# Kernel tuning notes

Hardware: AMD Instinct MI355X
Metric: run time of the kernel (lower is better)

Reference implementation:

```python
import jax, jax.numpy as jnp
import numpy as np

N_NODES = 50000
N_EDGES = 1600000
IN_CH = 128
HEADS = 4
HEAD_DIM = 32  # out_channels // heads = 128 // 4
NEG_SLOPE = 0.2


def setup_inputs() -> dict:
    key = jax.random.key(0)
    ks = jax.random.split(key, 6)
    x = jax.random.normal(ks[0], (N_NODES, IN_CH), dtype=jnp.float32)
    edge_index = jax.random.randint(ks[1], (2, N_EDGES), 0, N_NODES, dtype=jnp.int64)
    W = jax.random.normal(ks[2], (IN_CH, HEADS * HEAD_DIM), dtype=jnp.float32) * 0.1
    att_src = jax.random.normal(ks[3], (HEADS, HEAD_DIM), dtype=jnp.float32) * 0.1
    att_dst = jax.random.normal(ks[4], (HEADS, HEAD_DIM), dtype=jnp.float32) * 0.1
    bias = jax.random.normal(ks[5], (HEADS * HEAD_DIM,), dtype=jnp.float32) * 0.1
    return {"x": x, "edge_index": edge_index, "W": W,
            "att_src": att_src, "att_dst": att_dst, "bias": bias}


def reference(x, edge_index, W, att_src, att_dst, bias):
    N = x.shape[0]
    # linear projection, split heads: [N, H, C]
    h = (x @ W).reshape(N, HEADS, HEAD_DIM)
    # per-node attention logits: [N, H]
    a_src = jnp.einsum('nhc,hc->nh', h, att_src)
    a_dst = jnp.einsum('nhc,hc->nh', h, att_dst)
    # add self loops (PyG default)
    loops = jnp.arange(N, dtype=edge_index.dtype)
    src = jnp.concatenate([edge_index[0], loops])  # message source j
    dst = jnp.concatenate([edge_index[1], loops])  # message target i
    # edge attention scores: [E_total, H]
    alpha = jax.nn.leaky_relu(a_src[src] + a_dst[dst], NEG_SLOPE)
    # segment softmax over incoming edges per destination node
    amax = jax.ops.segment_max(alpha, dst, num_segments=N)
    alpha = jnp.exp(alpha - amax[dst])
    denom = jax.ops.segment_sum(alpha, dst, num_segments=N)
    alpha = alpha / (denom[dst] + 1e-16)
    # weighted scatter-aggregate: [N, H, C]
    msg = h[src] * alpha[:, :, None]
    out = jax.ops.segment_sum(msg, dst, num_segments=N)
    out = out.reshape(N, HEADS * HEAD_DIM) + bias
    return jax.nn.elu(out)
```

## Files before the change

### kernel.cpp

```cpp
#include <hip/hip_runtime.h>

typedef unsigned short u16;
typedef unsigned int u32;

#define CH 128
#define NHEAD 4
#define NEG_SLOPE 0.2f
#define ROWS_PER_BLOCK 32

#define LOG_NPB 7
#define NPB 128
#define NBMAX 400
#define BCAP 6144
#define KMAX 24
#define GPAD 16
#define BINA_BLOCKS 256

static __device__ __forceinline__ float bitf(u32 i) {
    float f; __builtin_memcpy(&f, &i, 4); return f;
}
static __device__ __forceinline__ float bflo(u32 v) { return bitf(v << 16); }
static __device__ __forceinline__ float bfhi(u32 v) { return bitf(v & 0xffff0000u); }
static __device__ __forceinline__ u16 f2bf(float f) {
    u32 i; __builtin_memcpy(&i, &f, 4);
    return (u16)((i + 0x7fffu + ((i >> 16) & 1u)) >> 16);
}
static __device__ __forceinline__ float lrelu(float v) { return v > 0.f ? v : NEG_SLOPE * v; }

static __device__ __forceinline__ int ei_at(const int* __restrict__ ei, int mode32, size_t idx) {
    return mode32 ? ei[idx] : ei[2 * idx];
}

__global__ __launch_bounds__(256) void gemmbin_kernel(
    const float* __restrict__ x, const float* __restrict__ W,
    const float* __restrict__ att_src, const float* __restrict__ att_dst,
    u16* __restrict__ h, float* __restrict__ asrc, float* __restrict__ adst, int N,
    const int* __restrict__ ei, int* __restrict__ gcur, u32* __restrict__ rec,
    int E, int NB)
{
    __shared__ u32 Wbf[CH][CH / 2];

    const int tid = threadIdx.x;

    if (blockIdx.x < BINA_BLOCKS) {
        int* hist  = (int*)&Wbf[0][0];
        int* hbase = hist + NBMAX;
        int* hcur  = hbase + NBMAX;
        const int mode32 = __syncthreads_or(ei[2 * tid + 1] != 0);
        for (int b = tid; b < NB; b += 256) { hist[b] = 0; hcur[b] = 0; }
        __syncthreads();
        const int chunk = (E + BINA_BLOCKS - 1) / BINA_BLOCKS;
        const int beg0 = blockIdx.x * chunk;
        const int end0 = min(E, beg0 + chunk);
#pragma unroll 4
        for (int e = beg0 + tid; e < end0; e += 256) {
            int dj = ei_at(ei, mode32, (size_t)E + e);
            atomicAdd(&hist[dj >> LOG_NPB], 1);
        }
        __syncthreads();
        for (int b = tid; b < NB; b += 256) {
            int c = hist[b];
            hbase[b] = c ? atomicAdd(&gcur[b * GPAD], c) : 0;
        }
        __syncthreads();
#pragma unroll 4
        for (int e = beg0 + tid; e < end0; e += 256) {
            int dj = ei_at(ei, mode32, (size_t)E + e);
            int sj = ei_at(ei, mode32, (size_t)e);
            int bkt = dj >> LOG_NPB;
            int r = atomicAdd(&hcur[bkt], 1);
            int pos = hbase[bkt] + r;
            if (pos < BCAP)
                rec[(size_t)bkt * BCAP + pos] = ((u32)sj << LOG_NPB) | (u32)(dj & (NPB - 1));
        }
        return;
    }

    const int gb = blockIdx.x - BINA_BLOCKS;
    const int r0b = gb * ROWS_PER_BLOCK;
#pragma unroll
    for (int i = 0; i < 16; ++i) {
        int f = tid + i * 256;
        int row = f >> 5;
        int col = (f & 31) * 4;
        float4 w4 = *(const float4*)(W + (size_t)row * CH + col);
        Wbf[row][(col >> 1)]     = (u32)f2bf(w4.x) | ((u32)f2bf(w4.y) << 16);
        Wbf[row][(col >> 1) + 1] = (u32)f2bf(w4.z) | ((u32)f2bf(w4.w) << 16);
    }
    __syncthreads();

    const int lane = tid & 63;
    const int wave = tid >> 6;
    const int c0 = lane * 2;
    const int head = lane >> 4;
    const float as0 = att_src[c0], as1 = att_src[c0 + 1];
    const float ad0 = att_dst[c0], ad1 = att_dst[c0 + 1];
    const int rwu = __builtin_amdgcn_readfirstlane(wave * 8);

    const float* xr[8];
#pragma unroll
    for (int r = 0; r < 8; ++r) {
        int row = r0b + rwu + r;
        row = row < N - 1 ? row : N - 1;
        xr[r] = x + (size_t)row * CH;
    }

    float acc[8][2];
#pragma unroll
    for (int r = 0; r < 8; ++r) { acc[r][0] = 0.f; acc[r][1] = 0.f; }

#pragma unroll 2
    for (int k4 = 0; k4 < 32; ++k4) {
        const int k = k4 * 4;
        u32 p0 = Wbf[k + 0][lane];
        u32 p1 = Wbf[k + 1][lane];
        u32 p2 = Wbf[k + 2][lane];
        u32 p3 = Wbf[k + 3][lane];
        float w00 = bflo(p0), w01 = bfhi(p0);
        float w10 = bflo(p1), w11 = bfhi(p1);
        float w20 = bflo(p2), w21 = bfhi(p2);
        float w30 = bflo(p3), w31 = bfhi(p3);
#pragma unroll
        for (int r = 0; r < 8; ++r) {
            float4 xv = *(const float4*)(xr[r] + k);
            acc[r][0] = fmaf(xv.x, w00, acc[r][0]);
            acc[r][1] = fmaf(xv.x, w01, acc[r][1]);
            acc[r][0] = fmaf(xv.y, w10, acc[r][0]);
            acc[r][1] = fmaf(xv.y, w11, acc[r][1]);
            acc[r][0] = fmaf(xv.z, w20, acc[r][0]);
            acc[r][1] = fmaf(xv.z, w21, acc[r][1]);
            acc[r][0] = fmaf(xv.w, w30, acc[r][0]);
            acc[r][1] = fmaf(xv.w, w31, acc[r][1]);
        }
    }
#pragma unroll
    for (int r = 0; r < 8; ++r) {
        int row = r0b + rwu + r;
        float sdot = acc[r][0] * as0 + acc[r][1] * as1;
        float ddot = acc[r][0] * ad0 + acc[r][1] * ad1;
#pragma unroll
        for (int o = 1; o < 16; o <<= 1) {
            sdot += __shfl_xor(sdot, o, 64);
            ddot += __shfl_xor(ddot, o, 64);
        }
        if (row < N) {
            u32 hp = (u32)f2bf(acc[r][0]) | ((u32)f2bf(acc[r][1]) << 16);
            *(u32*)(h + (size_t)row * CH + c0) = hp;
            if ((lane & 15) == 0) {
                asrc[row * NHEAD + head] = sdot;
                adst[row * NHEAD + head] = ddot;
            }
        }
    }
}

__global__ __launch_bounds__(256) void binB_kernel(
    const int* __restrict__ gcur, const u32* __restrict__ rec,
    int* __restrict__ csr, int* __restrict__ begA, int* __restrict__ degA, int N)
{
    __shared__ int outb[BCAP];
    __shared__ int lcnt[NPB];
    __shared__ int lsc[NPB];
    __shared__ int lcur[NPB];
    const int tid = threadIdx.x;
    const int bkt = blockIdx.x;
    int cnt0 = gcur[bkt * GPAD];
    cnt0 = cnt0 < BCAP ? cnt0 : BCAP;
    const size_t rbase = (size_t)bkt * BCAP;

    if (tid < NPB) { lcnt[tid] = 0; lcur[tid] = 0; }

    u32 rc[KMAX];
#pragma unroll
    for (int k = 0; k < KMAX; ++k) {
        int i = tid + k * 256;
        rc[k] = (i < cnt0) ? rec[rbase + i] : 0xffffffffu;
    }
    __syncthreads();
#pragma unroll
    for (int k = 0; k < KMAX; ++k)
        if (rc[k] != 0xffffffffu) atomicAdd(&lcnt[rc[k] & (NPB - 1)], 1);
    __syncthreads();
    if (tid < NPB) lsc[tid] = lcnt[tid];
    __syncthreads();
    for (int o = 1; o < NPB; o <<= 1) {
        int v = (tid < NPB && tid >= o) ? lsc[tid - o] : 0;
        __syncthreads();
        if (tid < NPB) lsc[tid] += v;
        __syncthreads();
    }
#pragma unroll
    for (int k = 0; k < KMAX; ++k) {
        if (rc[k] != 0xffffffffu) {
            int local = rc[k] & (NPB - 1);
            int r = atomicAdd(&lcur[local], 1);
            int slot = (lsc[local] - lcnt[local]) + r;
            outb[slot] = (int)(rc[k] >> LOG_NPB);
        }
    }
    __syncthreads();
    for (int i = tid; i < cnt0; i += 256)
        csr[rbase + i] = outb[i];
    if (tid < NPB) {
        int node = (bkt << LOG_NPB) + tid;
        if (node < N) {
            begA[node] = (int)rbase + (lsc[tid] - lcnt[tid]);
            degA[node] = lcnt[tid];
        }
    }
}

__global__ __launch_bounds__(256) void agg_kernel(
    const u16* __restrict__ h, const float* __restrict__ asrc, const float* __restrict__ adst,
    const int* __restrict__ begA, const int* __restrict__ degA, const int* __restrict__ csr,
    const float* __restrict__ bias, float* __restrict__ out, int N)
{
    const int lane = threadIdx.x & 63;
    const int wave = threadIdx.x >> 6;
    const int node = blockIdx.x * 4 + wave;
    if (node >= N) return;
    const int g = lane >> 4;
    const int l = lane & 15;
    const int c8 = l * 8;
    const int head = l >> 2;
    const int beg = begA[node];
    const int end = beg + degA[node];
    const float4 ad4 = *(const float4*)(adst + node * 4);
    const float adh = (head == 0) ? ad4.x : (head == 1) ? ad4.y : (head == 2) ? ad4.z : ad4.w;
    const float4 asl = *(const float4*)(asrc + node * 4);
    const float aslh = (head == 0) ? asl.x : (head == 1) ? asl.y : (head == 2) ? asl.z : asl.w;
    const float mh = lrelu(aslh + adh);

    float acc[8];
#pragma unroll
    for (int k = 0; k < 8; ++k) acc[k] = 0.f;
    float s = 0.f;

    int e = beg + g;
    if (e < end) {
        uint4 hC[4]; float aC[4];
#pragma unroll
        for (int i = 0; i < 4; ++i) {
            int ei = e + 4 * i;
            int j = csr[ei];
            j = ((u32)j < (u32)N) ? j : 0;
            float a = asrc[j * NHEAD + head];
            aC[i] = (ei < end) ? a : -1e30f;
            hC[i] = *(const uint4*)(h + (size_t)j * CH + c8);
        }
        for (;;) {
            const int ebase = e + 16;
            uint4 hP[4]; float aP[4];
#pragma unroll
            for (int i = 0; i < 4; ++i) {
                int ei = ebase + 4 * i;
                int j = csr[ei];
                j = ((u32)j < (u32)N) ? j : 0;
                float a = asrc[j * NHEAD + head];
                aP[i] = (ei < end) ? a : -1e30f;
                hP[i] = *(const uint4*)(h + (size_t)j * CH + c8);
            }
#pragma unroll
            for (int i = 0; i < 4; ++i) {
                float w = __expf(lrelu(aC[i] + adh) - mh);
                s += w;
                acc[0] = fmaf(w, bflo(hC[i].x), acc[0]);
                acc[1] = fmaf(w, bfhi(hC[i].x), acc[1]);
                acc[2] = fmaf(w, bflo(hC[i].y), acc[2]);
                acc[3] = fmaf(w, bfhi(hC[i].y), acc[3]);
                acc[4] = fmaf(w, bflo(hC[i].z), acc[4]);
                acc[5] = fmaf(w, bfhi(hC[i].z), acc[5]);
                acc[6] = fmaf(w, bflo(hC[i].w), acc[6]);
                acc[7] = fmaf(w, bfhi(hC[i].w), acc[7]);
            }
#pragma unroll
            for (int i = 0; i < 4; ++i) { aC[i] = aP[i]; hC[i] = hP[i]; }
            e = ebase;
            if (e >= end) break;
        }
    }
    if (g == 0) {
        s += 1.0f;
        uint4 hv = *(const uint4*)(h + (size_t)node * CH + c8);
        acc[0] += bflo(hv.x);
        acc[1] += bfhi(hv.x);
        acc[2] += bflo(hv.y);
        acc[3] += bfhi(hv.y);
        acc[4] += bflo(hv.z);
        acc[5] += bfhi(hv.z);
        acc[6] += bflo(hv.w);
        acc[7] += bfhi(hv.w);
    }
#pragma unroll
    for (int o = 16; o < 64; o <<= 1) {
        s += __shfl_xor(s, o, 64);
#pragma unroll
        for (int k = 0; k < 8; ++k) acc[k] += __shfl_xor(acc[k], o, 64);
    }
    if (g == 0) {
        const float inv = 1.f / (s + 1e-16f);
        float o0[8];
#pragma unroll
        for (int k = 0; k < 8; ++k) {
            float v = acc[k] * inv + bias[c8 + k];
            o0[k] = v > 0.f ? v : __expf(v) - 1.f;
        }
        float4 lo = make_float4(o0[0], o0[1], o0[2], o0[3]);
        float4 hi = make_float4(o0[4], o0[5], o0[6], o0[7]);
        *(float4*)(out + (size_t)node * CH + c8) = lo;
        *(float4*)(out + (size_t)node * CH + c8 + 4) = hi;
    }
}

extern "C" void kernel_launch(void* const* d_in, const int* in_sizes, int n_in,
                              void* d_out, int out_size, void* d_ws, size_t ws_size,
                              hipStream_t stream)
{
    const float* x       = (const float*)d_in[0];
    const int*   ei      = (const int*)d_in[1];
    const float* W       = (const float*)d_in[2];
    const float* att_src = (const float*)d_in[3];
    const float* att_dst = (const float*)d_in[4];
    const float* bias    = (const float*)d_in[5];
    float* out = (float*)d_out;
    const int N = in_sizes[0] / CH;
    const int E = in_sizes[1] / 2;
    const int NB = (N + NPB - 1) / NPB;

    char* p = (char*)d_ws;
    auto alloc = [&](size_t bytes) { char* r = p; p += (bytes + 255) & ~(size_t)255; return r; };
    u16*   h    = (u16*)alloc((size_t)N * CH * 2);
    float* asrc = (float*)alloc((size_t)N * NHEAD * 4);
    float* adst = (float*)alloc((size_t)N * NHEAD * 4);
    int*   gcur = (int*)alloc((size_t)NB * GPAD * 4);
    u32*   rec  = (u32*)alloc((size_t)NB * BCAP * 4);
    int*   csr  = (int*)alloc((size_t)NB * BCAP * 4 + 256);
    int*   begA = (int*)alloc((size_t)N * 4);
    int*   degA = (int*)alloc((size_t)N * 4);

    const int gemmBlocks = (N + ROWS_PER_BLOCK - 1) / ROWS_PER_BLOCK;
    hipMemsetAsync(gcur, 0, (size_t)NB * GPAD * 4, stream);
    gemmbin_kernel<<<BINA_BLOCKS + gemmBlocks, 256, 0, stream>>>(
        x, W, att_src, att_dst, h, asrc, adst, N, ei, gcur, rec, E, NB);
    binB_kernel<<<NB, 256, 0, stream>>>(gcur, rec, csr, begA, degA, N);
    agg_kernel<<<(N + 3) / 4, 256, 0, stream>>>(h, asrc, adst, begA, degA, csr, bias, out, N);
}
```

Before: 201.9 us.

## Pair GEMM with bin phase B instead of A; stage x rows in LDS

Moves bin phase A into its own kernel and merges the GEMM blocks into the same launch as bin phase B, with the two sharing LDS through a union. The GEMM now loads its 32-row x tile into shared memory before computing, rather than reading float4s straight from global memory in the inner loop, and the k-loop unroll goes from 2 to 4. The aim is to rebalance which work runs concurrently and to cut redundant global x reads. In exchange, LDS per block grows to about 48KB, which may lower occupancy, and the kernel count stays the same.

```diff
diff --git a/kernel.cpp b/kernel.cpp
--- a/kernel.cpp
+++ b/kernel.cpp
@@ -31,61 +31,131 @@
     return mode32 ? ei[idx] : ei[2 * idx];
 }
 
-__global__ __launch_bounds__(256) void gemmbin_kernel(
+__global__ __launch_bounds__(256) void binA_kernel(
+    const int* __restrict__ ei, int* __restrict__ gcur, u32* __restrict__ rec,
+    int E, int NB)
+{
+    __shared__ int hist[NBMAX];
+    __shared__ int hbase[NBMAX];
+    __shared__ int hcur[NBMAX];
+    const int tid = threadIdx.x;
+    const int mode32 = __syncthreads_or(ei[2 * tid + 1] != 0);
+    for (int b = tid; b < NB; b += 256) { hist[b] = 0; hcur[b] = 0; }
+    __syncthreads();
+    const int chunk = (E + BINA_BLOCKS - 1) / BINA_BLOCKS;
+    const int beg0 = blockIdx.x * chunk;
+    const int end0 = min(E, beg0 + chunk);
+#pragma unroll 4
+    for (int e = beg0 + tid; e < end0; e += 256) {
+        int dj = ei_at(ei, mode32, (size_t)E + e);
+        atomicAdd(&hist[dj >> LOG_NPB], 1);
+    }
+    __syncthreads();
+    for (int b = tid; b < NB; b += 256) {
+        int c = hist[b];
+        hbase[b] = c ? atomicAdd(&gcur[b * GPAD], c) : 0;
+    }
+    __syncthreads();
+#pragma unroll 4
+    for (int e = beg0 + tid; e < end0; e += 256) {
+        int dj = ei_at(ei, mode32, (size_t)E + e);
+        int sj = ei_at(ei, mode32, (size_t)e);
+        int bkt = dj >> LOG_NPB;
+        int r = atomicAdd(&hcur[bkt], 1);
+        int pos = hbase[bkt] + r;
+        if (pos < BCAP)
+            rec[(size_t)bkt * BCAP + pos] = ((u32)sj << LOG_NPB) | (u32)(dj & (NPB - 1));
+    }
+}
+
+union SMem {
+    struct { float xs[ROWS_PER_BLOCK][CH]; u32 Wbf[CH][CH / 2]; } g;
+    struct { int outb[BCAP]; int lcnt[NPB]; int lsc[NPB]; int lcur[NPB]; } b;
+};
+
+__global__ __launch_bounds__(256) void gemmbinB_kernel(
     const float* __restrict__ x, const float* __restrict__ W,
     const float* __restrict__ att_src, const float* __restrict__ att_dst,
     u16* __restrict__ h, float* __restrict__ asrc, float* __restrict__ adst, int N,
-    const int* __restrict__ ei, int* __restrict__ gcur, u32* __restrict__ rec,
-    int E, int NB)
+    const int* __restrict__ gcur, const u32* __restrict__ rec,
+    int* __restrict__ csr, int* __restrict__ begA, int* __restrict__ degA, int NB)
 {
-    __shared__ u32 Wbf[CH][CH / 2];
-
+    __shared__ SMem sm;
     const int tid = threadIdx.x;
 
-    if (blockIdx.x < BINA_BLOCKS) {
-        int* hist  = (int*)&Wbf[0][0];
-        int* hbase = hist + NBMAX;
-        int* hcur  = hbase + NBMAX;
-        const int mode32 = __syncthreads_or(ei[2 * tid + 1] != 0);
-        for (int b = tid; b < NB; b += 256) { hist[b] = 0; hcur[b] = 0; }
+    if ((int)blockIdx.x < NB) {
+        int* outb = sm.b.outb;
+        int* lcnt = sm.b.lcnt;
+        int* lsc  = sm.b.lsc;
+        int* lcur = sm.b.lcur;
+        const int bkt = blockIdx.x;
+        int cnt0 = gcur[bkt * GPAD];
+        cnt0 = cnt0 < BCAP ? cnt0 : BCAP;
+        const size_t rbase = (size_t)bkt * BCAP;
+
+        if (tid < NPB) { lcnt[tid] = 0; lcur[tid] = 0; }
+
+        u32 rc[KMAX];
+#pragma unroll
+        for (int k = 0; k < KMAX; ++k) {
+            int i = tid + k * 256;
+            rc[k] = (i < cnt0) ? rec[rbase + i] : 0xffffffffu;
+        }
         __syncthreads();
-        const int chunk = (E + BINA_BLOCKS - 1) / BINA_BLOCKS;
-        const int beg0 = blockIdx.x * chunk;
-        const int end0 = min(E, beg0 + chunk);
-#pragma unroll 4
-        for (int e = beg0 + tid; e < end0; e += 256) {
-            int dj = ei_at(ei, mode32, (size_t)E + e);
-            atomicAdd(&hist[dj >> LOG_NPB], 1);
-        }
+#pragma unroll
+        for (int k = 0; k < KMAX; ++k)
+            if (rc[k] != 0xffffffffu) atomicAdd(&lcnt[rc[k] & (NPB - 1)], 1);
         __syncthreads();
-        for (int b = tid; b < NB; b += 256) {
-            int c = hist[b];
-            hbase[b] = c ? atomicAdd(&gcur[b * GPAD], c) : 0;
-        }
+        if (tid < NPB) lsc[tid] = lcnt[tid];
         __syncthreads();
-#pragma unroll 4
-        for (int e = beg0 + tid; e < end0; e += 256) {
-            int dj = ei_at(ei, mode32, (size_t)E + e);
-            int sj = ei_at(ei, mode32, (size_t)e);
-            int bkt = dj >> LOG_NPB;
-            int r = atomicAdd(&hcur[bkt], 1);
-            int pos = hbase[bkt] + r;
-            if (pos < BCAP)
-                rec[(size_t)bkt * BCAP + pos] = ((u32)sj << LOG_NPB) | (u32)(dj & (NPB - 1));
+        for (int o = 1; o < NPB; o <<= 1) {
+            int v = (tid < NPB && tid >= o) ? lsc[tid - o] : 0;
+            __syncthreads();
+            if (tid < NPB) lsc[tid] += v;
+            __syncthreads();
+        }
+#pragma unroll
+        for (int k = 0; k < KMAX; ++k) {
+            if (rc[k] != 0xffffffffu) {
+                int local = rc[k] & (NPB - 1);
+                int r = atomicAdd(&lcur[local], 1);
+                int slot = (lsc[local] - lcnt[local]) + r;
+                outb[slot] = (int)(rc[k] >> LOG_NPB);
+            }
+        }
+        __syncthreads();
+        for (int i = tid; i < cnt0; i += 256)
+            csr[rbase + i] = outb[i];
+        if (tid < NPB) {
+            int node = (bkt << LOG_NPB) + tid;
+            if (node < N) {
+                begA[node] = (int)rbase + (lsc[tid] - lcnt[tid]);
+                degA[node] = lcnt[tid];
+            }
         }
         return;
     }
 
-    const int gb = blockIdx.x - BINA_BLOCKS;
+    const int gb = blockIdx.x - NB;
     const int r0b = gb * ROWS_PER_BLOCK;
-#pragma unroll
-    for (int i = 0; i < 16; ++i) {
-        int f = tid + i * 256;
-        int row = f >> 5;
-        int col = (f & 31) * 4;
-        float4 w4 = *(const float4*)(W + (size_t)row * CH + col);
-        Wbf[row][(col >> 1)]     = (u32)f2bf(w4.x) | ((u32)f2bf(w4.y) << 16);
-        Wbf[row][(col >> 1) + 1] = (u32)f2bf(w4.z) | ((u32)f2bf(w4.w) << 16);
+    {
+#pragma unroll
+        for (int i = 0; i < 16; ++i) {
+            int f = tid + i * 256;
+            int row = f >> 5;
+            int col = (f & 31) * 4;
+            float4 w4 = *(const float4*)(W + (size_t)row * CH + col);
+            sm.g.Wbf[row][(col >> 1)]     = (u32)f2bf(w4.x) | ((u32)f2bf(w4.y) << 16);
+            sm.g.Wbf[row][(col >> 1) + 1] = (u32)f2bf(w4.z) | ((u32)f2bf(w4.w) << 16);
+        }
+#pragma unroll
+        for (int i = 0; i < 4; ++i) {
+            int f = tid + i * 256;
+            int row = f >> 5;
+            int col = (f & 31) * 4;
+            if (r0b + row < N)
+                *(float4*)&sm.g.xs[row][col] = *(const float4*)(x + (size_t)(r0b + row) * CH + col);
+        }
     }
     __syncthreads();
 
@@ -95,34 +165,26 @@
     const int head = lane >> 4;
     const float as0 = att_src[c0], as1 = att_src[c0 + 1];
     const float ad0 = att_dst[c0], ad1 = att_dst[c0 + 1];
-    const int rwu = __builtin_amdgcn_readfirstlane(wave * 8);
-
-    const float* xr[8];
-#pragma unroll
-    for (int r = 0; r < 8; ++r) {
-        int row = r0b + rwu + r;
-        row = row < N - 1 ? row : N - 1;
-        xr[r] = x + (size_t)row * CH;
-    }
+    const int rw = wave * 8;
 
     float acc[8][2];
 #pragma unroll
     for (int r = 0; r < 8; ++r) { acc[r][0] = 0.f; acc[r][1] = 0.f; }
 
-#pragma unroll 2
+#pragma unroll 4
     for (int k4 = 0; k4 < 32; ++k4) {
         const int k = k4 * 4;
-        u32 p0 = Wbf[k + 0][lane];
-        u32 p1 = Wbf[k + 1][lane];
-        u32 p2 = Wbf[k + 2][lane];
-        u32 p3 = Wbf[k + 3][lane];
+        u32 p0 = sm.g.Wbf[k + 0][lane];
+        u32 p1 = sm.g.Wbf[k + 1][lane];
+        u32 p2 = sm.g.Wbf[k + 2][lane];
+        u32 p3 = sm.g.Wbf[k + 3][lane];
         float w00 = bflo(p0), w01 = bfhi(p0);
         float w10 = bflo(p1), w11 = bfhi(p1);
         float w20 = bflo(p2), w21 = bfhi(p2);
         float w30 = bflo(p3), w31 = bfhi(p3);
 #pragma unroll
         for (int r = 0; r < 8; ++r) {
-            float4 xv = *(const float4*)(xr[r] + k);
+            float4 xv = *(const float4*)&sm.g.xs[rw + r][k];
             acc[r][0] = fmaf(xv.x, w00, acc[r][0]);
             acc[r][1] = fmaf(xv.x, w01, acc[r][1]);
             acc[r][0] = fmaf(xv.y, w10, acc[r][0]);
@@ -135,7 +197,7 @@
     }
 #pragma unroll
     for (int r = 0; r < 8; ++r) {
-        int row = r0b + rwu + r;
+        int row = r0b + rw + r;
         float sdot = acc[r][0] * as0 + acc[r][1] * as1;
         float ddot = acc[r][0] * ad0 + acc[r][1] * ad1;
 #pragma unroll
@@ -150,62 +212,6 @@
                 asrc[row * NHEAD + head] = sdot;
                 adst[row * NHEAD + head] = ddot;
             }
-        }
-    }
-}
-
-__global__ __launch_bounds__(256) void binB_kernel(
-    const int* __restrict__ gcur, const u32* __restrict__ rec,
-    int* __restrict__ csr, int* __restrict__ begA, int* __restrict__ degA, int N)
-{
-    __shared__ int outb[BCAP];
-    __shared__ int lcnt[NPB];
-    __shared__ int lsc[NPB];
-    __shared__ int lcur[NPB];
-    const int tid = threadIdx.x;
-    const int bkt = blockIdx.x;
-    int cnt0 = gcur[bkt * GPAD];
-    cnt0 = cnt0 < BCAP ? cnt0 : BCAP;
-    const size_t rbase = (size_t)bkt * BCAP;
-
-    if (tid < NPB) { lcnt[tid] = 0; lcur[tid] = 0; }
-
-    u32 rc[KMAX];
-#pragma unroll
-    for (int k = 0; k < KMAX; ++k) {
-        int i = tid + k * 256;
-        rc[k] = (i < cnt0) ? rec[rbase + i] : 0xffffffffu;
-    }
-    __syncthreads();
-#pragma unroll
-    for (int k = 0; k < KMAX; ++k)
-        if (rc[k] != 0xffffffffu) atomicAdd(&lcnt[rc[k] & (NPB - 1)], 1);
-    __syncthreads();
-    if (tid < NPB) lsc[tid] = lcnt[tid];
-    __syncthreads();
-    for (int o = 1; o < NPB; o <<= 1) {
-        int v = (tid < NPB && tid >= o) ? lsc[tid - o] : 0;
-        __syncthreads();
-        if (tid < NPB) lsc[tid] += v;
-        __syncthreads();
-    }
-#pragma unroll
-    for (int k = 0; k < KMAX; ++k) {
-        if (rc[k] != 0xffffffffu) {
-            int local = rc[k] & (NPB - 1);
-            int r = atomicAdd(&lcur[local], 1);
-            int slot = (lsc[local] - lcnt[local]) + r;
-            outb[slot] = (int)(rc[k] >> LOG_NPB);
-        }
-    }
-    __syncthreads();
-    for (int i = tid; i < cnt0; i += 256)
-        csr[rbase + i] = outb[i];
-    if (tid < NPB) {
-        int node = (bkt << LOG_NPB) + tid;
-        if (node < N) {
-            begA[node] = (int)rbase + (lsc[tid] - lcnt[tid]);
-            degA[node] = lcnt[tid];
         }
     }
 }
@@ -340,8 +346,8 @@
 
     const int gemmBlocks = (N + ROWS_PER_BLOCK - 1) / ROWS_PER_BLOCK;
     hipMemsetAsync(gcur, 0, (size_t)NB * GPAD * 4, stream);
-    gemmbin_kernel<<<BINA_BLOCKS + gemmBlocks, 256, 0, stream>>>(
-        x, W, att_src, att_dst, h, asrc, adst, N, ei, gcur, rec, E, NB);
-    binB_kernel<<<NB, 256, 0, stream>>>(gcur, rec, csr, begA, degA, N);
+    binA_kernel<<<BINA_BLOCKS, 256, 0, stream>>>(ei, gcur, rec, E, NB);
+    gemmbinB_kernel<<<NB + gemmBlocks, 256, 0, stream>>>(
+        x, W, att_src, att_dst, h, asrc, adst, N, gcur, rec, csr, begA, degA, NB);
     agg_kernel<<<(N + 3) / 4, 256, 0, stream>>>(h, asrc, adst, begA, degA, csr, bias, out, N);
 }
```

After: 220.0 us. +9.0%, slower.

## Fuse bucket sort with aggregation in one kernel and stage x tiles in LDS

Applied to the files above, without the earlier changes.

The per-bucket CSR build and the attention aggregation now run in a single 1024-thread kernel. The sorted neighbor list stays in shared memory and each wave aggregates 8 nodes of the bucket, so the csr/begA/degA round trip through global memory and one launch go away. The GEMM also stages its 32 input rows of x in LDS instead of reading them directly from global memory. The trade-off is that only about 391 blocks run the aggregation, which lowers parallelism and load balance compared with the previous one-wave-per-node launch of 12500 blocks.

```diff
diff --git a/kernel.cpp b/kernel.cpp
--- a/kernel.cpp
+++ b/kernel.cpp
@@ -12,7 +12,7 @@
 #define NPB 128
 #define NBMAX 400
 #define BCAP 6144
-#define KMAX 24
+#define KMB 6
 #define GPAD 16
 #define BINA_BLOCKS 256
 
@@ -38,12 +38,13 @@
     const int* __restrict__ ei, int* __restrict__ gcur, u32* __restrict__ rec,
     int E, int NB)
 {
+    __shared__ float xs[ROWS_PER_BLOCK][CH];
     __shared__ u32 Wbf[CH][CH / 2];
 
     const int tid = threadIdx.x;
 
     if (blockIdx.x < BINA_BLOCKS) {
-        int* hist  = (int*)&Wbf[0][0];
+        int* hist  = (int*)&xs[0][0];
         int* hbase = hist + NBMAX;
         int* hcur  = hbase + NBMAX;
         const int mode32 = __syncthreads_or(ei[2 * tid + 1] != 0);
@@ -78,14 +79,24 @@
 
     const int gb = blockIdx.x - BINA_BLOCKS;
     const int r0b = gb * ROWS_PER_BLOCK;
-#pragma unroll
-    for (int i = 0; i < 16; ++i) {
-        int f = tid + i * 256;
-        int row = f >> 5;
-        int col = (f & 31) * 4;
-        float4 w4 = *(const float4*)(W + (size_t)row * CH + col);
-        Wbf[row][(col >> 1)]     = (u32)f2bf(w4.x) | ((u32)f2bf(w4.y) << 16);
-        Wbf[row][(col >> 1) + 1] = (u32)f2bf(w4.z) | ((u32)f2bf(w4.w) << 16);
+    {
+#pragma unroll
+        for (int i = 0; i < 16; ++i) {
+            int f = tid + i * 256;
+            int row = f >> 5;
+            int col = (f & 31) * 4;
+            float4 w4 = *(const float4*)(W + (size_t)row * CH + col);
+            Wbf[row][(col >> 1)]     = (u32)f2bf(w4.x) | ((u32)f2bf(w4.y) << 16);
+            Wbf[row][(col >> 1) + 1] = (u32)f2bf(w4.z) | ((u32)f2bf(w4.w) << 16);
+        }
+#pragma unroll
+        for (int i = 0; i < 4; ++i) {
+            int f = tid + i * 256;
+            int row = f >> 5;
+            int col = (f & 31) * 4;
+            if (r0b + row < N)
+                *(float4*)&xs[row][col] = *(const float4*)(x + (size_t)(r0b + row) * CH + col);
+        }
     }
     __syncthreads();
 
@@ -95,21 +106,13 @@
     const int head = lane >> 4;
     const float as0 = att_src[c0], as1 = att_src[c0 + 1];
     const float ad0 = att_dst[c0], ad1 = att_dst[c0 + 1];
-    const int rwu = __builtin_amdgcn_readfirstlane(wave * 8);
-
-    const float* xr[8];
-#pragma unroll
-    for (int r = 0; r < 8; ++r) {
-        int row = r0b + rwu + r;
-        row = row < N - 1 ? row : N - 1;
-        xr[r] = x + (size_t)row * CH;
-    }
+    const int rw = wave * 8;
 
     float acc[8][2];
 #pragma unroll
     for (int r = 0; r < 8; ++r) { acc[r][0] = 0.f; acc[r][1] = 0.f; }
 
-#pragma unroll 2
+#pragma unroll 4
     for (int k4 = 0; k4 < 32; ++k4) {
         const int k = k4 * 4;
         u32 p0 = Wbf[k + 0][lane];
@@ -122,7 +125,7 @@
         float w30 = bflo(p3), w31 = bfhi(p3);
 #pragma unroll
         for (int r = 0; r < 8; ++r) {
-            float4 xv = *(const float4*)(xr[r] + k);
+            float4 xv = *(const float4*)&xs[rw + r][k];
             acc[r][0] = fmaf(xv.x, w00, acc[r][0]);
             acc[r][1] = fmaf(xv.x, w01, acc[r][1]);
             acc[r][0] = fmaf(xv.y, w10, acc[r][0]);
@@ -135,7 +138,7 @@
     }
 #pragma unroll
     for (int r = 0; r < 8; ++r) {
-        int row = r0b + rwu + r;
+        int row = r0b + rw + r;
         float sdot = acc[r][0] * as0 + acc[r][1] * as1;
         float ddot = acc[r][0] * ad0 + acc[r][1] * ad1;
 #pragma unroll
@@ -154,11 +157,12 @@
     }
 }
 
-__global__ __launch_bounds__(256) void binB_kernel(
+__global__ __launch_bounds__(1024) void binBagg_kernel(
+    const u16* __restrict__ h, const float* __restrict__ asrc, const float* __restrict__ adst,
     const int* __restrict__ gcur, const u32* __restrict__ rec,
-    int* __restrict__ csr, int* __restrict__ begA, int* __restrict__ degA, int N)
+    const float* __restrict__ bias, float* __restrict__ out, int N)
 {
-    __shared__ int outb[BCAP];
+    __shared__ int outb[BCAP + 32];
     __shared__ int lcnt[NPB];
     __shared__ int lsc[NPB];
     __shared__ int lcur[NPB];
@@ -170,15 +174,15 @@
 
     if (tid < NPB) { lcnt[tid] = 0; lcur[tid] = 0; }
 
-    u32 rc[KMAX];
-#pragma unroll
-    for (int k = 0; k < KMAX; ++k) {
-        int i = tid + k * 256;
+    u32 rc[KMB];
+#pragma unroll
+    for (int k = 0; k < KMB; ++k) {
+        int i = tid + k * 1024;
         rc[k] = (i < cnt0) ? rec[rbase + i] : 0xffffffffu;
     }
     __syncthreads();
 #pragma unroll
-    for (int k = 0; k < KMAX; ++k)
+    for (int k = 0; k < KMB; ++k)
         if (rc[k] != 0xffffffffu) atomicAdd(&lcnt[rc[k] & (NPB - 1)], 1);
     __syncthreads();
     if (tid < NPB) lsc[tid] = lcnt[tid];
@@ -190,7 +194,7 @@
         __syncthreads();
     }
 #pragma unroll
-    for (int k = 0; k < KMAX; ++k) {
+    for (int k = 0; k < KMB; ++k) {
         if (rc[k] != 0xffffffffu) {
             int local = rc[k] & (NPB - 1);
             int r = atomicAdd(&lcur[local], 1);
@@ -199,116 +203,105 @@
         }
     }
     __syncthreads();
-    for (int i = tid; i < cnt0; i += 256)
-        csr[rbase + i] = outb[i];
-    if (tid < NPB) {
-        int node = (bkt << LOG_NPB) + tid;
-        if (node < N) {
-            begA[node] = (int)rbase + (lsc[tid] - lcnt[tid]);
-            degA[node] = lcnt[tid];
-        }
-    }
-}
-
-__global__ __launch_bounds__(256) void agg_kernel(
-    const u16* __restrict__ h, const float* __restrict__ asrc, const float* __restrict__ adst,
-    const int* __restrict__ begA, const int* __restrict__ degA, const int* __restrict__ csr,
-    const float* __restrict__ bias, float* __restrict__ out, int N)
-{
-    const int lane = threadIdx.x & 63;
-    const int wave = threadIdx.x >> 6;
-    const int node = blockIdx.x * 4 + wave;
-    if (node >= N) return;
+
+    const int lane = tid & 63;
+    const int wave = tid >> 6;
     const int g = lane >> 4;
     const int l = lane & 15;
     const int c8 = l * 8;
     const int head = l >> 2;
-    const int beg = begA[node];
-    const int end = beg + degA[node];
-    const float4 ad4 = *(const float4*)(adst + node * 4);
-    const float adh = (head == 0) ? ad4.x : (head == 1) ? ad4.y : (head == 2) ? ad4.z : ad4.w;
-    const float4 asl = *(const float4*)(asrc + node * 4);
-    const float aslh = (head == 0) ? asl.x : (head == 1) ? asl.y : (head == 2) ? asl.z : asl.w;
-    const float mh = lrelu(aslh + adh);
-
-    float acc[8];
-#pragma unroll
-    for (int k = 0; k < 8; ++k) acc[k] = 0.f;
-    float s = 0.f;
-
-    int e = beg + g;
-    if (e < end) {
-        uint4 hC[4]; float aC[4];
-#pragma unroll
-        for (int i = 0; i < 4; ++i) {
-            int ei = e + 4 * i;
-            int j = csr[ei];
-            j = ((u32)j < (u32)N) ? j : 0;
-            float a = asrc[j * NHEAD + head];
-            aC[i] = (ei < end) ? a : -1e30f;
-            hC[i] = *(const uint4*)(h + (size_t)j * CH + c8);
-        }
-        for (;;) {
-            const int ebase = e + 16;
-            uint4 hP[4]; float aP[4];
+
+    for (int nl = 0; nl < 8; ++nl) {
+        const int local = wave * 8 + nl;
+        const int node = (bkt << LOG_NPB) + local;
+        if (node >= N) continue;
+        const int beg = lsc[local] - lcnt[local];
+        const int end = lsc[local];
+        const float4 ad4 = *(const float4*)(adst + node * 4);
+        const float adh = (head == 0) ? ad4.x : (head == 1) ? ad4.y : (head == 2) ? ad4.z : ad4.w;
+        const float4 asl = *(const float4*)(asrc + node * 4);
+        const float aslh = (head == 0) ? asl.x : (head == 1) ? asl.y : (head == 2) ? asl.z : asl.w;
+        const float mh = lrelu(aslh + adh);
+
+        float acc[8];
+#pragma unroll
+        for (int k = 0; k < 8; ++k) acc[k] = 0.f;
+        float s = 0.f;
+
+        int e = beg + g;
+        if (e < end) {
+            uint4 hC[4]; float aC[4];
 #pragma unroll
             for (int i = 0; i < 4; ++i) {
-                int ei = ebase + 4 * i;
-                int j = csr[ei];
+                int ei = e + 4 * i;
+                int j = outb[ei];
                 j = ((u32)j < (u32)N) ? j : 0;
                 float a = asrc[j * NHEAD + head];
-                aP[i] = (ei < end) ? a : -1e30f;
-                hP[i] = *(const uint4*)(h + (size_t)j * CH + c8);
+                aC[i] = (ei < end) ? a : -1e30f;
+                hC[i] = *(const uint4*)(h + (size_t)j * CH + c8);
             }
-#pragma unroll
-            for (int i = 0; i < 4; ++i) {
-                float w = __expf(lrelu(aC[i] + adh) - mh);
-                s += w;
-                acc[0] = fmaf(w, bflo(hC[i].x), acc[0]);
-                acc[1] = fmaf(w, bfhi(hC[i].x), acc[1]);
-                acc[2] = fmaf(w, bflo(hC[i].y), acc[2]);
-                acc[3] = fmaf(w, bfhi(hC[i].y), acc[3]);
-                acc[4] = fmaf(w, bflo(hC[i].z), acc[4]);
-                acc[5] = fmaf(w, bfhi(hC[i].z), acc[5]);
-                acc[6] = fmaf(w, bflo(hC[i].w), acc[6]);
-                acc[7] = fmaf(w, bfhi(hC[i].w), acc[7]);
+            for (;;) {
+                const int ebase = e + 16;
+                uint4 hP[4]; float aP[4];
+#pragma unroll
+                for (int i = 0; i < 4; ++i) {
+                    int ei = ebase + 4 * i;
+                    int j = outb[ei];
+                    j = ((u32)j < (u32)N) ? j : 0;
+                    float a = asrc[j * NHEAD + head];
+                    aP[i] = (ei < end) ? a : -1e30f;
+                    hP[i] = *(const uint4*)(h + (size_t)j * CH + c8);
+                }
+#pragma unroll
+                for (int i = 0; i < 4; ++i) {
+                    float w = __expf(lrelu(aC[i] + adh) - mh);
+                    s += w;
+                    acc[0] = fmaf(w, bflo(hC[i].x), acc[0]);
+                    acc[1] = fmaf(w, bfhi(hC[i].x), acc[1]);
+                    acc[2] = fmaf(w, bflo(hC[i].y), acc[2]);
+                    acc[3] = fmaf(w, bfhi(hC[i].y), acc[3]);
+                    acc[4] = fmaf(w, bflo(hC[i].z), acc[4]);
+                    acc[5] = fmaf(w, bfhi(hC[i].z), acc[5]);
+                    acc[6] = fmaf(w, bflo(hC[i].w), acc[6]);
+                    acc[7] = fmaf(w, bfhi(hC[i].w), acc[7]);
+                }
+#pragma unroll
+                for (int i = 0; i < 4; ++i) { aC[i] = aP[i]; hC[i] = hP[i]; }
+                e = ebase;
+                if (e >= end) break;
             }
-#pragma unroll
-            for (int i = 0; i < 4; ++i) { aC[i] = aP[i]; hC[i] = hP[i]; }
-            e = ebase;
-            if (e >= end) break;
-        }
-    }
-    if (g == 0) {
-        s += 1.0f;
-        uint4 hv = *(const uint4*)(h + (size_t)node * CH + c8);
-        acc[0] += bflo(hv.x);
-        acc[1] += bfhi(hv.x);
-        acc[2] += bflo(hv.y);
-        acc[3] += bfhi(hv.y);
-        acc[4] += bflo(hv.z);
-        acc[5] += bfhi(hv.z);
-        acc[6] += bflo(hv.w);
-        acc[7] += bfhi(hv.w);
-    }
-#pragma unroll
-    for (int o = 16; o < 64; o <<= 1) {
-        s += __shfl_xor(s, o, 64);
-#pragma unroll
-        for (int k = 0; k < 8; ++k) acc[k] += __shfl_xor(acc[k], o, 64);
-    }
-    if (g == 0) {
-        const float inv = 1.f / (s + 1e-16f);
-        float o0[8];
-#pragma unroll
-        for (int k = 0; k < 8; ++k) {
-            float v = acc[k] * inv + bias[c8 + k];
-            o0[k] = v > 0.f ? v : __expf(v) - 1.f;
-        }
-        float4 lo = make_float4(o0[0], o0[1], o0[2], o0[3]);
-        float4 hi = make_float4(o0[4], o0[5], o0[6], o0[7]);
-        *(float4*)(out + (size_t)node * CH + c8) = lo;
-        *(float4*)(out + (size_t)node * CH + c8 + 4) = hi;
+        }
+        if (g == 0) {
+            s += 1.0f;
+            uint4 hv = *(const uint4*)(h + (size_t)node * CH + c8);
+            acc[0] += bflo(hv.x);
+            acc[1] += bfhi(hv.x);
+            acc[2] += bflo(hv.y);
+            acc[3] += bfhi(hv.y);
+            acc[4] += bflo(hv.z);
+            acc[5] += bfhi(hv.z);
+            acc[6] += bflo(hv.w);
+            acc[7] += bfhi(hv.w);
+        }
+#pragma unroll
+        for (int o = 16; o < 64; o <<= 1) {
+            s += __shfl_xor(s, o, 64);
+#pragma unroll
+            for (int k = 0; k < 8; ++k) acc[k] += __shfl_xor(acc[k], o, 64);
+        }
+        if (g == 0) {
+            const float inv = 1.f / (s + 1e-16f);
+            float o0[8];
+#pragma unroll
+            for (int k = 0; k < 8; ++k) {
+                float v = acc[k] * inv + bias[c8 + k];
+                o0[k] = v > 0.f ? v : __expf(v) - 1.f;
+            }
+            float4 lo = make_float4(o0[0], o0[1], o0[2], o0[3]);
+            float4 hi = make_float4(o0[4], o0[5], o0[6], o0[7]);
+            *(float4*)(out + (size_t)node * CH + c8) = lo;
+            *(float4*)(out + (size_t)node * CH + c8 + 4) = hi;
+        }
     }
 }
 
@@ -334,14 +327,10 @@
     float* adst = (float*)alloc((size_t)N * NHEAD * 4);
     int*   gcur = (int*)alloc((size_t)NB * GPAD * 4);
     u32*   rec  = (u32*)alloc((size_t)NB * BCAP * 4);
-    int*   csr  = (int*)alloc((size_t)NB * BCAP * 4 + 256);
-    int*   begA = (int*)alloc((size_t)N * 4);
-    int*   degA = (int*)alloc((size_t)N * 4);
 
     const int gemmBlocks = (N + ROWS_PER_BLOCK - 1) / ROWS_PER_BLOCK;
     hipMemsetAsync(gcur, 0, (size_t)NB * GPAD * 4, stream);
     gemmbin_kernel<<<BINA_BLOCKS + gemmBlocks, 256, 0, stream>>>(
         x, W, att_src, att_dst, h, asrc, adst, N, ei, gcur, rec, E, NB);
-    binB_kernel<<<NB, 256, 0, stream>>>(gcur, rec, csr, begA, degA, N);
-    agg_kernel<<<(N + 3) / 4, 256, 0, stream>>>(h, asrc, adst, begA, degA, csr, bias, out, N);
-}
+    binBagg_kernel<<<NB, 1024, 0, stream>>>(h, asrc, adst, gcur, rec, bias, out, N);
+}
```

New measurement: 200.5 us. No clear change (-0.7%).
